# Kernel tuning notes

Measured on AMD Instinct MI355X. Metric: run time of the kernel, lower is better.

The kernel has to match this reference:

```python
import jax, jax.numpy as jnp
import numpy as np

N = 100000   # nodes
E = 3200000  # edges
D = 128      # in_channels
H = 128      # subhiddens
O = 128      # out_channels
S = 2048     # subgraphs
EPS = 1e-5


def _glorot(k, shape):
    lim = np.sqrt(6.0 / (shape[0] + shape[1])).astype(np.float32)
    return jax.random.uniform(k, shape, jnp.float32, -lim, lim)


def setup_inputs() -> dict:
    key = jax.random.key(0)
    ks = jax.random.split(key, 8)
    x = jax.random.normal(ks[0], (N, D), jnp.float32)
    edge_index = jax.random.randint(ks[1], (2, E), 0, N, dtype=jnp.int32)
    node_to_subgraph = jnp.sort(jax.random.randint(ks[2], (N,), 0, S, dtype=jnp.int32))
    return {
        "x": x,
        "edge_index": edge_index,
        "node_to_subgraph": node_to_subgraph,
        "W1": _glorot(ks[3], (D, H)), "b1": jnp.zeros((H,), jnp.float32),
        "g1": jnp.ones((H,), jnp.float32), "be1": jnp.zeros((H,), jnp.float32),
        "W2": _glorot(ks[4], (H, H)), "b2": jnp.zeros((H,), jnp.float32),
        "g2": jnp.ones((H,), jnp.float32), "be2": jnp.zeros((H,), jnp.float32),
        "W3": _glorot(ks[5], (H, O)), "b3": jnp.zeros((O,), jnp.float32),
    }


def _gcn_conv(x, W, b, row, col, norm):
    # PyG GCNConv: out[col] += norm * (x @ W)[row], then + bias.
    xw = x @ W                                    # [N+?, d] -> [N, d_out]
    msg = xw[row] * norm[:, None]                 # gather over source nodes
    out = jax.ops.segment_sum(msg, col, num_segments=N)
    return out + b


def _bn_relu(x, g, be):
    # BatchNorm1d (training-mode batch stats, biased var) + ReLU
    mean = jnp.mean(x, axis=0)
    var = jnp.mean(jnp.square(x - mean), axis=0)
    return jax.nn.relu((x - mean) * jax.lax.rsqrt(var + EPS) * g + be)


def reference(x, edge_index, node_to_subgraph, W1, b1, g1, be1, W2, b2, g2, be2, W3, b3):
    # GCN symmetric norm with self-loops, shared across the 3 convs.
    loops = jnp.arange(N, dtype=edge_index.dtype)
    row = jnp.concatenate([edge_index[0], loops])  # source
    col = jnp.concatenate([edge_index[1], loops])  # target (aggregation)
    deg = jax.ops.segment_sum(jnp.ones_like(col, dtype=x.dtype), col, num_segments=N)
    dinv = jnp.where(deg > 0, jax.lax.rsqrt(deg), 0.0)
    norm = dinv[row] * dinv[col]

    h1 = _bn_relu(_gcn_conv(x, W1, b1, row, col, norm), g1, be1)   # dropout is no-op in eval
    h2 = _bn_relu(_gcn_conv(h1, W2, b2, row, col, norm), g2, be2)
    h3 = jax.nn.relu(_gcn_conv(h2, W3, b3, row, col, norm))

    cat = jnp.concatenate([h1, h2, h3], axis=-1)                   # [N, 2H+O]
    return jax.ops.segment_max(cat, node_to_subgraph, num_segments=S)  # gmp -> [S, 2H+O]
```

## Files before the change

kernel.cpp:

```cpp
#include <hip/hip_runtime.h>
#include <hip/hip_fp16.h>

#define NN 100000
#define NE 3200000
#define DF 128
#define SG 2048
#define OUTC 384
#define EPS 1e-5f

#define NBUK 800
#define BNODES 125
#define CAP 5120
#define TILE 8192
#define LDSTRIDE 136

typedef _Float16 f16x8 __attribute__((ext_vector_type(8)));
typedef float f32x16 __attribute__((ext_vector_type(16)));

__global__ void k_prepW(const float* __restrict__ W1, const float* __restrict__ W2,
                        const float* __restrict__ W3, __half* __restrict__ WT) {
    const float* W = blockIdx.x == 0 ? W1 : (blockIdx.x == 1 ? W2 : W3);
    __half* out = WT + blockIdx.x * 16384;
    for (int i = threadIdx.x; i < 16384; i += 256) {
        int k = i >> 7, n = i & 127;
        out[n * 128 + k] = __float2half(W[i]);
    }
}

__global__ __launch_bounds__(256) void k_bucketA(const int* __restrict__ erow,
                                                 const int* __restrict__ ecol,
                                                 int* __restrict__ gcur,
                                                 int* __restrict__ packed) {
    __shared__ int hist[1024];
    __shared__ int loff[1024];
    __shared__ int gch[1024];
    __shared__ int cur[1024];
    __shared__ int psum[256];
    int t = threadIdx.x;
    hist[t] = 0; hist[t + 256] = 0; hist[t + 512] = 0; hist[t + 768] = 0;
    __syncthreads();
    int e0 = blockIdx.x * TILE;
    for (int i = t; i < TILE && e0 + i < NE; i += 256) {
        int c = ecol[e0 + i];
        atomicAdd(&hist[c / BNODES], 1);
    }
    __syncthreads();
    int h0 = hist[4 * t], h1 = hist[4 * t + 1], h2 = hist[4 * t + 2], h3 = hist[4 * t + 3];
    int s = h0 + h1 + h2 + h3;
    psum[t] = s; __syncthreads();
    for (int st = 1; st < 256; st <<= 1) {
        int a = (t >= st) ? psum[t - st] : 0;
        __syncthreads();
        psum[t] += a;
        __syncthreads();
    }
    int base = psum[t] - s;
    loff[4 * t] = base;
    loff[4 * t + 1] = base + h0;
    loff[4 * t + 2] = base + h0 + h1;
    loff[4 * t + 3] = base + h0 + h1 + h2;
#pragma unroll
    for (int j = 0; j < 4; ++j) {
        int b = 4 * t + j;
        if (b < NBUK) {
            int c = hist[b];
            gch[b] = c ? atomicAdd(&gcur[b], c) : 0;
            cur[b] = loff[b];
        }
    }
    __syncthreads();
    for (int i = t; i < TILE && e0 + i < NE; i += 256) {
        int c = ecol[e0 + i];
        int r = erow[e0 + i];
        int b = c / BNODES;
        int lc = c - b * BNODES;
        int p = atomicAdd(&cur[b], 1);
        int rank = p - loff[b];
        if (gch[b] + rank < CAP) packed[b * CAP + gch[b] + rank] = r | (lc << 17);
    }
}

__global__ __launch_bounds__(256) void k_csrB(int* __restrict__ rows,
                                              const int* __restrict__ gcur,
                                              int* __restrict__ begs, int* __restrict__ ends,
                                              float* __restrict__ dinv) {
    __shared__ int lin[CAP];
    __shared__ int hist[128], off[128], cur[128], psc[128];
    int b = blockIdx.x, t = threadIdx.x;
    int cnt = gcur[b]; if (cnt > CAP) cnt = CAP;
    int base = b * CAP;
    for (int i = t; i < cnt; i += 256) lin[i] = rows[base + i];
    if (t < 128) hist[t] = 0;
    __syncthreads();
    for (int i = t; i < cnt; i += 256) atomicAdd(&hist[lin[i] >> 17], 1);
    __syncthreads();
    int pc = 0;
    if (t < 128) { pc = (hist[t] + 3) & ~3; psc[t] = pc; }
    __syncthreads();
    for (int st = 1; st < 128; st <<= 1) {
        int a = 0;
        if (t < 128 && t >= st) a = psc[t - st];
        __syncthreads();
        if (t < 128) psc[t] += a;
        __syncthreads();
    }
    if (t < 128) { off[t] = psc[t] - pc; cur[t] = off[t]; }
    __syncthreads();
    if (t < BNODES) {
        int n = b * BNODES + t;
        int c = hist[t];
        int bg = base + off[t];
        begs[n] = bg;
        ends[n] = bg + c;
        dinv[n] = rsqrtf((float)(c + 1));
        int pad = (c + 3) & ~3;
        for (int p = c; p < pad; ++p)
            if (off[t] + p < CAP) rows[base + off[t] + p] = 0;
    }
    __syncthreads();
    for (int i = t; i < cnt; i += 256) {
        int w = lin[i];
        int lc = w >> 17;
        int p = atomicAdd(&cur[lc], 1);
        if (p < CAP) rows[base + p] = w & 0x1FFFF;
    }
}

__global__ __launch_bounds__(256, 2) void k_gemm16(const __half* __restrict__ A,
                                                   const __half* __restrict__ WTg,
                                                   const float* __restrict__ dinv,
                                                   __half* __restrict__ C) {
    __shared__ _Float16 Wl[128 * LDSTRIDE];
    int tid = threadIdx.x;
    for (int ch = tid; ch < 2048; ch += 256) {
        int n = ch >> 4, seg = ch & 15;
        *(uint4*)&Wl[n * LDSTRIDE + seg * 8] = *(const uint4*)(WTg + n * 128 + seg * 8);
    }
    __syncthreads();
    int wave = tid >> 6, lane = tid & 63;
    int l31 = lane & 31, lhi = lane >> 5;
    int rowbase = blockIdx.x * 256 + wave * 64;
    f32x16 acc[2][4];
#pragma unroll
    for (int rt = 0; rt < 2; ++rt)
#pragma unroll
        for (int nt = 0; nt < 4; ++nt)
#pragma unroll
            for (int i = 0; i < 16; ++i) acc[rt][nt][i] = 0.f;
    int r0 = rowbase + l31;      if (r0 >= NN) r0 = NN - 1;
    int r1 = rowbase + 32 + l31; if (r1 >= NN) r1 = NN - 1;
    const f16x8* A0 = (const f16x8*)(A + (size_t)r0 * 128);
    const f16x8* A1 = (const f16x8*)(A + (size_t)r1 * 128);
#pragma unroll
    for (int ks = 0; ks < 8; ++ks) {
        f16x8 a0 = A0[ks * 2 + lhi];
        f16x8 a1 = A1[ks * 2 + lhi];
#pragma unroll
        for (int nt = 0; nt < 4; ++nt) {
            f16x8 b = *(const f16x8*)&Wl[(nt * 32 + l31) * LDSTRIDE + ks * 16 + lhi * 8];
            acc[0][nt] = __builtin_amdgcn_mfma_f32_32x32x16_f16(a0, b, acc[0][nt], 0, 0, 0);
            acc[1][nt] = __builtin_amdgcn_mfma_f32_32x32x16_f16(a1, b, acc[1][nt], 0, 0, 0);
        }
    }
#pragma unroll
    for (int rt = 0; rt < 2; ++rt) {
#pragma unroll
        for (int r = 0; r < 16; ++r) {
            int row = rowbase + rt * 32 + (r & 3) + 8 * (r >> 2) + 4 * lhi;
            if (row < NN) {
                float sc = dinv[row];
                size_t cb = (size_t)row * 128 + l31;
                C[cb]      = __float2half(acc[rt][0][r] * sc);
                C[cb + 32] = __float2half(acc[rt][1][r] * sc);
                C[cb + 64] = __float2half(acc[rt][2][r] * sc);
                C[cb + 96] = __float2half(acc[rt][3][r] * sc);
            }
        }
    }
}

__global__ __launch_bounds__(256, 2) void k_gemm32(const float* __restrict__ A,
                                                   const __half* __restrict__ WTg,
                                                   const float* __restrict__ dinv,
                                                   __half* __restrict__ C) {
    __shared__ _Float16 Wl[128 * LDSTRIDE];
    int tid = threadIdx.x;
    for (int ch = tid; ch < 2048; ch += 256) {
        int n = ch >> 4, seg = ch & 15;
        *(uint4*)&Wl[n * LDSTRIDE + seg * 8] = *(const uint4*)(WTg + n * 128 + seg * 8);
    }
    __syncthreads();
    int wave = tid >> 6, lane = tid & 63;
    int l31 = lane & 31, lhi = lane >> 5;
    int rowbase = blockIdx.x * 256 + wave * 64;
    f32x16 acc[2][4];
#pragma unroll
    for (int rt = 0; rt < 2; ++rt)
#pragma unroll
        for (int nt = 0; nt < 4; ++nt)
#pragma unroll
            for (int i = 0; i < 16; ++i) acc[rt][nt][i] = 0.f;
    int r0 = rowbase + l31;      if (r0 >= NN) r0 = NN - 1;
    int r1 = rowbase + 32 + l31; if (r1 >= NN) r1 = NN - 1;
    const float* A0 = A + (size_t)r0 * 128;
    const float* A1 = A + (size_t)r1 * 128;
#pragma unroll
    for (int ks = 0; ks < 8; ++ks) {
        int koff = ks * 16 + lhi * 8;
        float4 f0 = *(const float4*)(A0 + koff);
        float4 f1 = *(const float4*)(A0 + koff + 4);
        float4 g0 = *(const float4*)(A1 + koff);
        float4 g1 = *(const float4*)(A1 + koff + 4);
        f16x8 a0, a1;
        a0[0] = (_Float16)f0.x; a0[1] = (_Float16)f0.y; a0[2] = (_Float16)f0.z; a0[3] = (_Float16)f0.w;
        a0[4] = (_Float16)f1.x; a0[5] = (_Float16)f1.y; a0[6] = (_Float16)f1.z; a0[7] = (_Float16)f1.w;
        a1[0] = (_Float16)g0.x; a1[1] = (_Float16)g0.y; a1[2] = (_Float16)g0.z; a1[3] = (_Float16)g0.w;
        a1[4] = (_Float16)g1.x; a1[5] = (_Float16)g1.y; a1[6] = (_Float16)g1.z; a1[7] = (_Float16)g1.w;
#pragma unroll
        for (int nt = 0; nt < 4; ++nt) {
            f16x8 b = *(const f16x8*)&Wl[(nt * 32 + l31) * LDSTRIDE + ks * 16 + lhi * 8];
            acc[0][nt] = __builtin_amdgcn_mfma_f32_32x32x16_f16(a0, b, acc[0][nt], 0, 0, 0);
            acc[1][nt] = __builtin_amdgcn_mfma_f32_32x32x16_f16(a1, b, acc[1][nt], 0, 0, 0);
        }
    }
#pragma unroll
    for (int rt = 0; rt < 2; ++rt) {
#pragma unroll
        for (int r = 0; r < 16; ++r) {
            int row = rowbase + rt * 32 + (r & 3) + 8 * (r >> 2) + 4 * lhi;
            if (row < NN) {
                float sc = dinv[row];
                size_t cb = (size_t)row * 128 + l31;
                C[cb]      = __float2half(acc[rt][0][r] * sc);
                C[cb + 32] = __float2half(acc[rt][1][r] * sc);
                C[cb + 64] = __float2half(acc[rt][2][r] * sc);
                C[cb + 96] = __float2half(acc[rt][3][r] * sc);
            }
        }
    }
}

__device__ __forceinline__ void accum8(float* acc, uint4 v) {
    float2 f;
    f = __half22float2(*(__half2*)&v.x); acc[0] += f.x; acc[1] += f.y;
    f = __half22float2(*(__half2*)&v.y); acc[2] += f.x; acc[3] += f.y;
    f = __half22float2(*(__half2*)&v.z); acc[4] += f.x; acc[5] += f.y;
    f = __half22float2(*(__half2*)&v.w); acc[6] += f.x; acc[7] += f.y;
}
__device__ __forceinline__ void accum8w(float* acc, uint4 v, float w) {
    float2 f;
    f = __half22float2(*(__half2*)&v.x); acc[0] = fmaf(w, f.x, acc[0]); acc[1] = fmaf(w, f.y, acc[1]);
    f = __half22float2(*(__half2*)&v.y); acc[2] = fmaf(w, f.x, acc[2]); acc[3] = fmaf(w, f.y, acc[3]);
    f = __half22float2(*(__half2*)&v.z); acc[4] = fmaf(w, f.x, acc[4]); acc[5] = fmaf(w, f.y, acc[5]);
    f = __half22float2(*(__half2*)&v.w); acc[6] = fmaf(w, f.x, acc[6]); acc[7] = fmaf(w, f.y, acc[7]);
}

#define AGG_BLOCKS 4096
__global__ __launch_bounds__(256) void k_aggh(const __half* __restrict__ XWh,
                                              const int* __restrict__ begs,
                                              const int* __restrict__ ends,
                                              const int* __restrict__ rows,
                                              const float* __restrict__ dinv,
                                              __half* __restrict__ outh) {
    int wid = (blockIdx.x * 256 + threadIdx.x) >> 6;
    int lane = threadIdx.x & 63;
    int quad = lane >> 4, li = lane & 15;
    const uint4* XW4 = (const uint4*)XWh;
    for (int n = wid; n < NN; n += AGG_BLOCKS * 4) {
        float dn = dinv[n];
        int beg = begs[n], end = ends[n];
        float acc[8] = {};
        if (quad == 0) {
            uint4 sv = XW4[(size_t)n * 16 + li];
            accum8(acc, sv);
        }
        int e = beg;
        for (; e + 32 <= end; e += 32) {
            int4 ia = *(const int4*)(rows + e + 4 * quad);
            int4 ib = *(const int4*)(rows + e + 16 + 4 * quad);
            uint4 v0 = XW4[(size_t)ia.x * 16 + li];
            uint4 v1 = XW4[(size_t)ia.y * 16 + li];
            uint4 v2 = XW4[(size_t)ia.z * 16 + li];
            uint4 v3 = XW4[(size_t)ia.w * 16 + li];
            uint4 v4 = XW4[(size_t)ib.x * 16 + li];
            uint4 v5 = XW4[(size_t)ib.y * 16 + li];
            uint4 v6 = XW4[(size_t)ib.z * 16 + li];
            uint4 v7 = XW4[(size_t)ib.w * 16 + li];
            accum8(acc, v0); accum8(acc, v1); accum8(acc, v2); accum8(acc, v3);
            accum8(acc, v4); accum8(acc, v5); accum8(acc, v6); accum8(acc, v7);
        }
        for (; e + 16 <= end; e += 16) {
            int4 ia = *(const int4*)(rows + e + 4 * quad);
            uint4 v0 = XW4[(size_t)ia.x * 16 + li];
            uint4 v1 = XW4[(size_t)ia.y * 16 + li];
            uint4 v2 = XW4[(size_t)ia.z * 16 + li];
            uint4 v3 = XW4[(size_t)ia.w * 16 + li];
            accum8(acc, v0); accum8(acc, v1); accum8(acc, v2); accum8(acc, v3);
        }
        if (e < end) {
            int rem = end - e;
            int qb = 4 * quad;
            int4 it = make_int4(0, 0, 0, 0);
            if (qb < rem) it = *(const int4*)(rows + e + qb);
            uint4 v0 = XW4[(size_t)it.x * 16 + li];
            uint4 v1 = XW4[(size_t)it.y * 16 + li];
            uint4 v2 = XW4[(size_t)it.z * 16 + li];
            uint4 v3 = XW4[(size_t)it.w * 16 + li];
            accum8w(acc, v0, (qb + 0 < rem) ? 1.f : 0.f);
            accum8w(acc, v1, (qb + 1 < rem) ? 1.f : 0.f);
            accum8w(acc, v2, (qb + 2 < rem) ? 1.f : 0.f);
            accum8w(acc, v3, (qb + 3 < rem) ? 1.f : 0.f);
        }
#pragma unroll
        for (int j = 0; j < 8; ++j) {
            acc[j] += __shfl_xor(acc[j], 16, 64);
            acc[j] += __shfl_xor(acc[j], 32, 64);
        }
        if (quad == 0) {
            __half2 h0 = __floats2half2_rn(acc[0] * dn, acc[1] * dn);
            __half2 h1 = __floats2half2_rn(acc[2] * dn, acc[3] * dn);
            __half2 h2 = __floats2half2_rn(acc[4] * dn, acc[5] * dn);
            __half2 h3 = __floats2half2_rn(acc[6] * dn, acc[7] * dn);
            uint4 st;
            st.x = *(unsigned int*)&h0;
            st.y = *(unsigned int*)&h1;
            st.z = *(unsigned int*)&h2;
            st.w = *(unsigned int*)&h3;
            *(uint4*)(outh + (size_t)n * 128 + li * 8) = st;
        }
    }
}

__global__ void k_stats(const __half* __restrict__ buf, float* __restrict__ sums) {
    int c = threadIdx.x & 127;
    int rg = threadIdx.x >> 7;
    float s = 0.f, q = 0.f;
    for (int r = blockIdx.x * 2 + rg; r < NN; r += gridDim.x * 2) {
        float v = __half2float(buf[(size_t)r * 128 + c]);
        s += v; q += v * v;
    }
    __shared__ float sh[512];
    sh[threadIdx.x] = s;
    sh[256 + threadIdx.x] = q;
    __syncthreads();
    if (threadIdx.x < 128) {
        s = sh[threadIdx.x] + sh[threadIdx.x + 128];
        q = sh[256 + threadIdx.x] + sh[256 + threadIdx.x + 128];
        atomicAdd(&sums[threadIdx.x], s);
        atomicAdd(&sums[128 + threadIdx.x], q);
    }
}

__global__ void k_bnmax(__half* __restrict__ buf, const float* __restrict__ sums,
                        const float* __restrict__ g, const float* __restrict__ be,
                        const int* __restrict__ n2s,
                        unsigned int* __restrict__ outmax, int colOff) {
    int c = threadIdx.x & 127;
    int rg = threadIdx.x >> 7;
    int n0 = blockIdx.x * 64;
    int nEnd = n0 + 64; if (nEnd > NN) nEnd = NN;
    float mean = sums[c] * (1.0f / NN);
    float inv = rsqrtf(sums[128 + c] * (1.0f / NN) - mean * mean + EPS) * g[c];
    float sc = inv, sh = be[c] - mean * inv;
    int cur = -1; float runmax = 0.f;
    for (int n = n0 + rg; n < nEnd; n += 2) {
        float v = fmaxf(__half2float(buf[(size_t)n * 128 + c]) * sc + sh, 0.f);
        buf[(size_t)n * 128 + c] = __float2half(v);
        int sg = n2s[n];
        if (sg != cur) {
            if (cur >= 0) atomicMax(&outmax[cur * OUTC + colOff + c], __float_as_uint(runmax));
            cur = sg; runmax = v;
        } else {
            runmax = fmaxf(runmax, v);
        }
    }
    if (cur >= 0) atomicMax(&outmax[cur * OUTC + colOff + c], __float_as_uint(runmax));
}

__global__ void k_biasmax(const __half* __restrict__ buf, const float* __restrict__ b3,
                          const int* __restrict__ n2s,
                          unsigned int* __restrict__ outmax, int colOff) {
    int c = threadIdx.x & 127;
    int rg = threadIdx.x >> 7;
    int n0 = blockIdx.x * 64;
    int nEnd = n0 + 64; if (nEnd > NN) nEnd = NN;
    float bias = b3[c];
    int cur = -1; float runmax = 0.f;
    for (int n = n0 + rg; n < nEnd; n += 2) {
        float v = fmaxf(__half2float(buf[(size_t)n * 128 + c]) + bias, 0.f);
        int sg = n2s[n];
        if (sg != cur) {
            if (cur >= 0) atomicMax(&outmax[cur * OUTC + colOff + c], __float_as_uint(runmax));
            cur = sg; runmax = v;
        } else {
            runmax = fmaxf(runmax, v);
        }
    }
    if (cur >= 0) atomicMax(&outmax[cur * OUTC + colOff + c], __float_as_uint(runmax));
}

extern "C" void kernel_launch(void* const* d_in, const int* in_sizes, int n_in,
                              void* d_out, int out_size, void* d_ws, size_t ws_size,
                              hipStream_t stream) {
    const float* x   = (const float*)d_in[0];
    const int*   ei  = (const int*)d_in[1];
    const int*   n2s = (const int*)d_in[2];
    const float* W1  = (const float*)d_in[3];
    const float* g1  = (const float*)d_in[5];
    const float* be1 = (const float*)d_in[6];
    const float* W2  = (const float*)d_in[7];
    const float* g2  = (const float*)d_in[9];
    const float* be2 = (const float*)d_in[10];
    const float* W3  = (const float*)d_in[11];
    const float* b3  = (const float*)d_in[12];

    __half* H    = (__half*)d_ws;
    __half* XWh  = H + (size_t)NN * 128;
    __half* WT   = XWh + (size_t)NN * 128;
    int* rows    = (int*)(WT + 3 * 16384);
    int* begs    = rows + (size_t)NBUK * CAP;
    int* ends    = begs + NN;
    float* dinv  = (float*)(ends + NN);
    int* gcur    = (int*)(dinv + NN);
    float* sums  = (float*)(gcur + NBUK);

    const int* erow = ei;
    const int* ecol = ei + NE;

    hipMemsetAsync(gcur, 0, (NBUK + 512) * sizeof(int), stream);
    hipMemsetAsync(d_out, 0, (size_t)out_size * sizeof(float), stream);

    k_prepW<<<3, 256, 0, stream>>>(W1, W2, W3, WT);
    int nbA = (NE + TILE - 1) / TILE;
    k_bucketA<<<nbA, 256, 0, stream>>>(erow, ecol, gcur, rows);
    k_csrB<<<NBUK, 256, 0, stream>>>(rows, gcur, begs, ends, dinv);

    unsigned int* outmax = (unsigned int*)d_out;
    int nbSeg = (NN + 63) / 64;
    int nbG = (NN + 255) / 256;

    k_gemm32<<<nbG, 256, 0, stream>>>(x, WT, dinv, XWh);
    k_aggh<<<AGG_BLOCKS, 256, 0, stream>>>(XWh, begs, ends, rows, dinv, H);
    k_stats<<<512, 256, 0, stream>>>(H, sums);
    k_bnmax<<<nbSeg, 256, 0, stream>>>(H, sums, g1, be1, n2s, outmax, 0);

    k_gemm16<<<nbG, 256, 0, stream>>>(H, WT + 16384, dinv, XWh);
    k_aggh<<<AGG_BLOCKS, 256, 0, stream>>>(XWh, begs, ends, rows, dinv, H);
    k_stats<<<512, 256, 0, stream>>>(H, sums + 256);
    k_bnmax<<<nbSeg, 256, 0, stream>>>(H, sums + 256, g2, be2, n2s, outmax, 128);

    k_gemm16<<<nbG, 256, 0, stream>>>(H, WT + 32768, dinv, XWh);
    k_aggh<<<AGG_BLOCKS, 256, 0, stream>>>(XWh, begs, ends, rows, dinv, H);
    k_biasmax<<<nbSeg, 256, 0, stream>>>(H, b3, n2s, outmax, 256);
}
```

Measured before the change: 731.2 us.

## Fuse edge bucketing with first-layer GEMM in one launch, scale by source dinv

The edge-bucketing kernel and the first-layer fp32 GEMM become one launch whose blocks are split by index, so the GEMM can run alongside the bucketing instead of waiting for the CSR/dinv build. The first GEMM no longer scales by dinv. A new first-layer aggregation kernel instead gathers dinv per source edge, which adds extra random loads per edge. The bucketing tile is halved and stages edge data in LDS to avoid re-reading global memory, and the aggregation block count is halved.

```diff
diff --git a/kernel.cpp b/kernel.cpp
--- a/kernel.cpp
+++ b/kernel.cpp
@@ -11,8 +11,11 @@
 #define NBUK 800
 #define BNODES 125
 #define CAP 5120
-#define TILE 8192
+#define TILE 4096
+#define B_BUCKET 782
+#define B_GEMM 391
 #define LDSTRIDE 136
+#define AGG_BLOCKS 2048
 
 typedef _Float16 f16x8 __attribute__((ext_vector_type(8)));
 typedef float f32x16 __attribute__((ext_vector_type(16)));
@@ -27,21 +30,25 @@
     }
 }
 
-__global__ __launch_bounds__(256) void k_bucketA(const int* __restrict__ erow,
-                                                 const int* __restrict__ ecol,
-                                                 int* __restrict__ gcur,
-                                                 int* __restrict__ packed) {
-    __shared__ int hist[1024];
-    __shared__ int loff[1024];
-    __shared__ int gch[1024];
-    __shared__ int cur[1024];
-    __shared__ int psum[256];
+__device__ void bucketA_body(int* smem, int bb,
+                             const int* __restrict__ erow, const int* __restrict__ ecol,
+                             int* __restrict__ gcur, int* __restrict__ packed) {
+    int* sc   = smem;
+    int* sr   = smem + 4096;
+    int* hist = smem + 8192;
+    int* loff = smem + 9216;
+    int* gch  = smem + 10240;
+    int* cur  = smem + 11264;
+    int* psum = smem + 12288;
     int t = threadIdx.x;
     hist[t] = 0; hist[t + 256] = 0; hist[t + 512] = 0; hist[t + 768] = 0;
     __syncthreads();
-    int e0 = blockIdx.x * TILE;
-    for (int i = t; i < TILE && e0 + i < NE; i += 256) {
+    int e0 = bb * TILE;
+    int lim = NE - e0; if (lim > TILE) lim = TILE;
+    for (int i = t; i < lim; i += 256) {
         int c = ecol[e0 + i];
+        int r = erow[e0 + i];
+        sc[i] = c; sr[i] = r;
         atomicAdd(&hist[c / BNODES], 1);
     }
     __syncthreads();
@@ -69,15 +76,85 @@
         }
     }
     __syncthreads();
-    for (int i = t; i < TILE && e0 + i < NE; i += 256) {
-        int c = ecol[e0 + i];
-        int r = erow[e0 + i];
+    for (int i = t; i < lim; i += 256) {
+        int c = sc[i], r = sr[i];
         int b = c / BNODES;
         int lc = c - b * BNODES;
         int p = atomicAdd(&cur[b], 1);
         int rank = p - loff[b];
         if (gch[b] + rank < CAP) packed[b * CAP + gch[b] + rank] = r | (lc << 17);
     }
+}
+
+__device__ void gemm32u_body(int* smem, int gb, const float* __restrict__ A,
+                             const __half* __restrict__ WTg, __half* __restrict__ C) {
+    _Float16* Wl = (_Float16*)smem;
+    int tid = threadIdx.x;
+    for (int ch = tid; ch < 2048; ch += 256) {
+        int n = ch >> 4, seg = ch & 15;
+        *(uint4*)&Wl[n * LDSTRIDE + seg * 8] = *(const uint4*)(WTg + n * 128 + seg * 8);
+    }
+    __syncthreads();
+    int wave = tid >> 6, lane = tid & 63;
+    int l31 = lane & 31, lhi = lane >> 5;
+    int rowbase = gb * 256 + wave * 64;
+    f32x16 acc[2][4];
+#pragma unroll
+    for (int rt = 0; rt < 2; ++rt)
+#pragma unroll
+        for (int nt = 0; nt < 4; ++nt)
+#pragma unroll
+            for (int i = 0; i < 16; ++i) acc[rt][nt][i] = 0.f;
+    int r0 = rowbase + l31;      if (r0 >= NN) r0 = NN - 1;
+    int r1 = rowbase + 32 + l31; if (r1 >= NN) r1 = NN - 1;
+    const float* A0 = A + (size_t)r0 * 128;
+    const float* A1 = A + (size_t)r1 * 128;
+#pragma unroll
+    for (int ks = 0; ks < 8; ++ks) {
+        int koff = ks * 16 + lhi * 8;
+        float4 f0 = *(const float4*)(A0 + koff);
+        float4 f1 = *(const float4*)(A0 + koff + 4);
+        float4 g0 = *(const float4*)(A1 + koff);
+        float4 g1 = *(const float4*)(A1 + koff + 4);
+        f16x8 a0, a1;
+        a0[0] = (_Float16)f0.x; a0[1] = (_Float16)f0.y; a0[2] = (_Float16)f0.z; a0[3] = (_Float16)f0.w;
+        a0[4] = (_Float16)f1.x; a0[5] = (_Float16)f1.y; a0[6] = (_Float16)f1.z; a0[7] = (_Float16)f1.w;
+        a1[0] = (_Float16)g0.x; a1[1] = (_Float16)g0.y; a1[2] = (_Float16)g0.z; a1[3] = (_Float16)g0.w;
+        a1[4] = (_Float16)g1.x; a1[5] = (_Float16)g1.y; a1[6] = (_Float16)g1.z; a1[7] = (_Float16)g1.w;
+#pragma unroll
+        for (int nt = 0; nt < 4; ++nt) {
+            f16x8 b = *(const f16x8*)&Wl[(nt * 32 + l31) * LDSTRIDE + ks * 16 + lhi * 8];
+            acc[0][nt] = __builtin_amdgcn_mfma_f32_32x32x16_f16(a0, b, acc[0][nt], 0, 0, 0);
+            acc[1][nt] = __builtin_amdgcn_mfma_f32_32x32x16_f16(a1, b, acc[1][nt], 0, 0, 0);
+        }
+    }
+#pragma unroll
+    for (int rt = 0; rt < 2; ++rt) {
+#pragma unroll
+        for (int r = 0; r < 16; ++r) {
+            int row = rowbase + rt * 32 + (r & 3) + 8 * (r >> 2) + 4 * lhi;
+            if (row < NN) {
+                size_t cb = (size_t)row * 128 + l31;
+                C[cb]      = __float2half(acc[rt][0][r]);
+                C[cb + 32] = __float2half(acc[rt][1][r]);
+                C[cb + 64] = __float2half(acc[rt][2][r]);
+                C[cb + 96] = __float2half(acc[rt][3][r]);
+            }
+        }
+    }
+}
+
+__global__ __launch_bounds__(256, 2) void k_fused1(const int* __restrict__ erow,
+                                                   const int* __restrict__ ecol,
+                                                   int* __restrict__ gcur,
+                                                   int* __restrict__ packed,
+                                                   const float* __restrict__ x,
+                                                   const __half* __restrict__ WT,
+                                                   __half* __restrict__ XWh) {
+    __shared__ __align__(16) int smem[12544];
+    int bb = blockIdx.x;
+    if (bb < B_BUCKET) bucketA_body(smem, bb, erow, ecol, gcur, packed);
+    else gemm32u_body(smem, bb - B_BUCKET, x, WT, XWh);
 }
 
 __global__ __launch_bounds__(256) void k_csrB(int* __restrict__ rows,
@@ -179,67 +256,6 @@
     }
 }
 
-__global__ __launch_bounds__(256, 2) void k_gemm32(const float* __restrict__ A,
-                                                   const __half* __restrict__ WTg,
-                                                   const float* __restrict__ dinv,
-                                                   __half* __restrict__ C) {
-    __shared__ _Float16 Wl[128 * LDSTRIDE];
-    int tid = threadIdx.x;
-    for (int ch = tid; ch < 2048; ch += 256) {
-        int n = ch >> 4, seg = ch & 15;
-        *(uint4*)&Wl[n * LDSTRIDE + seg * 8] = *(const uint4*)(WTg + n * 128 + seg * 8);
-    }
-    __syncthreads();
-    int wave = tid >> 6, lane = tid & 63;
-    int l31 = lane & 31, lhi = lane >> 5;
-    int rowbase = blockIdx.x * 256 + wave * 64;
-    f32x16 acc[2][4];
-#pragma unroll
-    for (int rt = 0; rt < 2; ++rt)
-#pragma unroll
-        for (int nt = 0; nt < 4; ++nt)
-#pragma unroll
-            for (int i = 0; i < 16; ++i) acc[rt][nt][i] = 0.f;
-    int r0 = rowbase + l31;      if (r0 >= NN) r0 = NN - 1;
-    int r1 = rowbase + 32 + l31; if (r1 >= NN) r1 = NN - 1;
-    const float* A0 = A + (size_t)r0 * 128;
-    const float* A1 = A + (size_t)r1 * 128;
-#pragma unroll
-    for (int ks = 0; ks < 8; ++ks) {
-        int koff = ks * 16 + lhi * 8;
-        float4 f0 = *(const float4*)(A0 + koff);
-        float4 f1 = *(const float4*)(A0 + koff + 4);
-        float4 g0 = *(const float4*)(A1 + koff);
-        float4 g1 = *(const float4*)(A1 + koff + 4);
-        f16x8 a0, a1;
-        a0[0] = (_Float16)f0.x; a0[1] = (_Float16)f0.y; a0[2] = (_Float16)f0.z; a0[3] = (_Float16)f0.w;
-        a0[4] = (_Float16)f1.x; a0[5] = (_Float16)f1.y; a0[6] = (_Float16)f1.z; a0[7] = (_Float16)f1.w;
-        a1[0] = (_Float16)g0.x; a1[1] = (_Float16)g0.y; a1[2] = (_Float16)g0.z; a1[3] = (_Float16)g0.w;
-        a1[4] = (_Float16)g1.x; a1[5] = (_Float16)g1.y; a1[6] = (_Float16)g1.z; a1[7] = (_Float16)g1.w;
-#pragma unroll
-        for (int nt = 0; nt < 4; ++nt) {
-            f16x8 b = *(const f16x8*)&Wl[(nt * 32 + l31) * LDSTRIDE + ks * 16 + lhi * 8];
-            acc[0][nt] = __builtin_amdgcn_mfma_f32_32x32x16_f16(a0, b, acc[0][nt], 0, 0, 0);
-            acc[1][nt] = __builtin_amdgcn_mfma_f32_32x32x16_f16(a1, b, acc[1][nt], 0, 0, 0);
-        }
-    }
-#pragma unroll
-    for (int rt = 0; rt < 2; ++rt) {
-#pragma unroll
-        for (int r = 0; r < 16; ++r) {
-            int row = rowbase + rt * 32 + (r & 3) + 8 * (r >> 2) + 4 * lhi;
-            if (row < NN) {
-                float sc = dinv[row];
-                size_t cb = (size_t)row * 128 + l31;
-                C[cb]      = __float2half(acc[rt][0][r] * sc);
-                C[cb + 32] = __float2half(acc[rt][1][r] * sc);
-                C[cb + 64] = __float2half(acc[rt][2][r] * sc);
-                C[cb + 96] = __float2half(acc[rt][3][r] * sc);
-            }
-        }
-    }
-}
-
 __device__ __forceinline__ void accum8(float* acc, uint4 v) {
     float2 f;
     f = __half22float2(*(__half2*)&v.x); acc[0] += f.x; acc[1] += f.y;
@@ -255,7 +271,6 @@
     f = __half22float2(*(__half2*)&v.w); acc[6] = fmaf(w, f.x, acc[6]); acc[7] = fmaf(w, f.y, acc[7]);
 }
 
-#define AGG_BLOCKS 4096
 __global__ __launch_bounds__(256) void k_aggh(const __half* __restrict__ XWh,
                                               const int* __restrict__ begs,
                                               const int* __restrict__ ends,
@@ -310,6 +325,74 @@
             accum8w(acc, v1, (qb + 1 < rem) ? 1.f : 0.f);
             accum8w(acc, v2, (qb + 2 < rem) ? 1.f : 0.f);
             accum8w(acc, v3, (qb + 3 < rem) ? 1.f : 0.f);
+        }
+#pragma unroll
+        for (int j = 0; j < 8; ++j) {
+            acc[j] += __shfl_xor(acc[j], 16, 64);
+            acc[j] += __shfl_xor(acc[j], 32, 64);
+        }
+        if (quad == 0) {
+            __half2 h0 = __floats2half2_rn(acc[0] * dn, acc[1] * dn);
+            __half2 h1 = __floats2half2_rn(acc[2] * dn, acc[3] * dn);
+            __half2 h2 = __floats2half2_rn(acc[4] * dn, acc[5] * dn);
+            __half2 h3 = __floats2half2_rn(acc[6] * dn, acc[7] * dn);
+            uint4 st;
+            st.x = *(unsigned int*)&h0;
+            st.y = *(unsigned int*)&h1;
+            st.z = *(unsigned int*)&h2;
+            st.w = *(unsigned int*)&h3;
+            *(uint4*)(outh + (size_t)n * 128 + li * 8) = st;
+        }
+    }
+}
+
+__global__ __launch_bounds__(256) void k_aggh1(const __half* __restrict__ XWh,
+                                               const int* __restrict__ begs,
+                                               const int* __restrict__ ends,
+                                               const int* __restrict__ rows,
+                                               const float* __restrict__ dinv,
+                                               __half* __restrict__ outh) {
+    int wid = (blockIdx.x * 256 + threadIdx.x) >> 6;
+    int lane = threadIdx.x & 63;
+    int quad = lane >> 4, li = lane & 15;
+    const uint4* XW4 = (const uint4*)XWh;
+    for (int n = wid; n < NN; n += AGG_BLOCKS * 4) {
+        float dn = dinv[n];
+        int beg = begs[n], end = ends[n];
+        float acc[8] = {};
+        if (quad == 0) {
+            uint4 sv = XW4[(size_t)n * 16 + li];
+            accum8w(acc, sv, dn);
+        }
+        int e = beg;
+        for (; e + 16 <= end; e += 16) {
+            int4 ia = *(const int4*)(rows + e + 4 * quad);
+            float d0 = dinv[ia.x];
+            float d1 = dinv[ia.y];
+            float d2 = dinv[ia.z];
+            float d3 = dinv[ia.w];
+            uint4 v0 = XW4[(size_t)ia.x * 16 + li];
+            uint4 v1 = XW4[(size_t)ia.y * 16 + li];
+            uint4 v2 = XW4[(size_t)ia.z * 16 + li];
+            uint4 v3 = XW4[(size_t)ia.w * 16 + li];
+            accum8w(acc, v0, d0); accum8w(acc, v1, d1);
+            accum8w(acc, v2, d2); accum8w(acc, v3, d3);
+        }
+        if (e < end) {
+            int rem = end - e;
+            int qb = 4 * quad;
+            int4 it = make_int4(0, 0, 0, 0);
+            if (qb < rem) it = *(const int4*)(rows + e + qb);
+            float d0 = (qb + 0 < rem) ? dinv[it.x] : 0.f;
+            float d1 = (qb + 1 < rem) ? dinv[it.y] : 0.f;
+            float d2 = (qb + 2 < rem) ? dinv[it.z] : 0.f;
+            float d3 = (qb + 3 < rem) ? dinv[it.w] : 0.f;
+            uint4 v0 = XW4[(size_t)it.x * 16 + li];
+            uint4 v1 = XW4[(size_t)it.y * 16 + li];
+            uint4 v2 = XW4[(size_t)it.z * 16 + li];
+            uint4 v3 = XW4[(size_t)it.w * 16 + li];
+            accum8w(acc, v0, d0); accum8w(acc, v1, d1);
+            accum8w(acc, v2, d2); accum8w(acc, v3, d3);
         }
 #pragma unroll
         for (int j = 0; j < 8; ++j) {
@@ -431,16 +514,14 @@
     hipMemsetAsync(d_out, 0, (size_t)out_size * sizeof(float), stream);
 
     k_prepW<<<3, 256, 0, stream>>>(W1, W2, W3, WT);
-    int nbA = (NE + TILE - 1) / TILE;
-    k_bucketA<<<nbA, 256, 0, stream>>>(erow, ecol, gcur, rows);
+    k_fused1<<<B_BUCKET + B_GEMM, 256, 0, stream>>>(erow, ecol, gcur, rows, x, WT, XWh);
     k_csrB<<<NBUK, 256, 0, stream>>>(rows, gcur, begs, ends, dinv);
 
     unsigned int* outmax = (unsigned int*)d_out;
     int nbSeg = (NN + 63) / 64;
     int nbG = (NN + 255) / 256;
 
-    k_gemm32<<<nbG, 256, 0, stream>>>(x, WT, dinv, XWh);
-    k_aggh<<<AGG_BLOCKS, 256, 0, stream>>>(XWh, begs, ends, rows, dinv, H);
+    k_aggh1<<<AGG_BLOCKS, 256, 0, stream>>>(XWh, begs, ends, rows, dinv, H);
     k_stats<<<512, 256, 0, stream>>>(H, sums);
     k_bnmax<<<nbSeg, 256, 0, stream>>>(H, sums, g1, be1, n2s, outmax, 0);
 
```

Result: no change. 745.3 us (+1.9%).
